# Optimization experiments

Measured on AMD Instinct MI355X. Metric: run time of the kernel, lower is better.

Reference implementation:

```python
import jax, jax.numpy as jnp
import numpy as np


def setup_inputs() -> dict:
    key = jax.random.key(0)
    k1, k2 = jax.random.split(key)
    pred = jax.random.normal(k1, (16, 4096, 3), dtype=jnp.float32)
    target = jax.random.normal(k2, (16, 4096, 3), dtype=jnp.float32)
    return {"pred": pred, "target": target}


def _pairwise_l2(pc1, pc2):
    # pc1: (B,N,3), pc2: (B,M,3) -> (B,N,M) euclidean distances (torch.cdist p=2)
    sq1 = jnp.sum(pc1 * pc1, axis=-1)  # (B,N)
    sq2 = jnp.sum(pc2 * pc2, axis=-1)  # (B,M)
    inner = jnp.einsum("bnd,bmd->bnm", pc1, pc2)  # (B,N,M)
    d2 = sq1[:, :, None] + sq2[:, None, :] - 2.0 * inner
    return jnp.sqrt(jnp.maximum(d2, 0.0))


def reference(pred, target):
    d = _pairwise_l2(pred, target)          # (B,N,M)
    dist1 = jnp.mean(jnp.min(d, axis=2), axis=1)  # (B,) pred -> target
    dist2 = jnp.mean(jnp.min(d, axis=1), axis=1)  # (B,) target -> pred
    chamfer = (dist1 + dist2) / 2.0         # bidirectional=True
    return jnp.mean(chamfer)
```

## Files before the change

### kernel.cpp

```cpp
#include <hip/hip_runtime.h>
#include <math.h>
#include <stdint.h>


#define BATCH   16
#define NPTS    4096
#define THREADS 256
#define NITEMS  (2 * BATCH * NPTS)
#define MAIN_BLOCKS (2 * BATCH * (NPTS / 128))

typedef __attribute__((ext_vector_type(8)))  _Float16 half8;
typedef __attribute__((ext_vector_type(16))) float    floatx16;

union Pack16 { float4 f4; _Float16 h[8]; half8 h8; };

__global__ __launch_bounds__(256) void chamfer_prep(
    const float* __restrict__ pred, const float* __restrict__ target,
    float4* __restrict__ packP, float4* __restrict__ packT)
{
    int g = blockIdx.x * 256 + threadIdx.x;
    int arr = g >> 16;
    int pt  = g & 65535;
    const float* src = arr ? target : pred;
    float x = src[pt * 3 + 0];
    float y = src[pt * 3 + 1];
    float z = src[pt * 3 + 2];
    _Float16 hx = (_Float16)x, hy = (_Float16)y, hz = (_Float16)z;
    float xf = (float)hx, yf = (float)hy, zf = (float)hz;
    float t = xf * xf + yf * yf + zf * zf;
    _Float16 h1 = (_Float16)t;
    _Float16 h2 = (_Float16)(t - (float)h1);
    Pack16 p;
    p.h[0] = hx; p.h[1] = hy; p.h[2] = hz; p.h[3] = h1; p.h[4] = h2;
    p.h[5] = (_Float16)0.0f; p.h[6] = (_Float16)0.0f; p.h[7] = (_Float16)0.0f;
    (arr ? packT : packP)[pt] = p.f4;
}

__device__ inline half8 make_bfrag(const Pack16& praw, bool lo) {
    half8 f;
#pragma unroll
    for (int i = 0; i < 8; ++i) f[i] = (_Float16)0.0f;
    if (lo) {
        f[0] = (_Float16)(praw.h[0] * (_Float16)-2.0f);
        f[1] = (_Float16)(praw.h[1] * (_Float16)-2.0f);
        f[2] = (_Float16)(praw.h[2] * (_Float16)-2.0f);
        f[3] = (_Float16)1.0f;
        f[4] = (_Float16)1.0f;
    }
    return f;
}

__global__ __launch_bounds__(THREADS, 4) void chamfer_main(
    const float4* __restrict__ packP, const float4* __restrict__ packT,
    float* __restrict__ blocksum)
{
    __shared__ float pmin[4][64];
    __shared__ float wsum[2];

    int tid  = threadIdx.x;
    int lane = tid & 63;
    int wave = tid >> 6;
    int qhalf = wave & 1;
    int chalf = wave >> 1;
    int l31  = lane & 31;
    bool lo  = lane < 32;

    int id = blockIdx.x;
    int ng = id & 31; id >>= 5;
    int b  = id & 15; id >>= 4;
    int dir = id;

    const float4* qpack = dir ? packT : packP;
    const float4* cpack = dir ? packP : packT;

    size_t qbase = (size_t)b * NPTS + ng * 128 + qhalf * 64;
    Pack16 prA, prB;
    prA.f4 = qpack[qbase + l31];
    prB.f4 = qpack[qbase + 32 + l31];
    half8 bfragA = make_bfrag(prA, lo);
    half8 bfragB = make_bfrag(prB, lo);

    const float4* cb = cpack + (size_t)b * NPTS + chalf * 2048;

    floatx16 zero, mnA, mnB;
#pragma unroll
    for (int r = 0; r < 16; ++r) { zero[r] = 0.0f; mnA[r] = 1e30f; mnB[r] = 1e30f; }

#pragma unroll 2
    for (int t = 0; t < 32; ++t) {
        Pack16 a0, a1;
        a0.f4 = cb[t * 64 + l31];
        a1.f4 = cb[t * 64 + 32 + l31];
        floatx16 d0 = __builtin_amdgcn_mfma_f32_32x32x16_f16(a0.h8, bfragA, zero, 0, 0, 0);
        floatx16 d1 = __builtin_amdgcn_mfma_f32_32x32x16_f16(a0.h8, bfragB, zero, 0, 0, 0);
#pragma unroll
        for (int r = 0; r < 16; ++r) mnA[r] = fminf(d0[r], mnA[r]);
#pragma unroll
        for (int r = 0; r < 16; ++r) mnB[r] = fminf(d1[r], mnB[r]);
        floatx16 d2 = __builtin_amdgcn_mfma_f32_32x32x16_f16(a1.h8, bfragA, zero, 0, 0, 0);
        floatx16 d3 = __builtin_amdgcn_mfma_f32_32x32x16_f16(a1.h8, bfragB, zero, 0, 0, 0);
#pragma unroll
        for (int r = 0; r < 16; ++r) mnA[r] = fminf(d2[r], mnA[r]);
#pragma unroll
        for (int r = 0; r < 16; ++r) mnB[r] = fminf(d3[r], mnB[r]);
    }

    float mA = fminf(fminf(fminf(mnA[0], mnA[1]),   fminf(mnA[2], mnA[3])),
                     fminf(fminf(mnA[4], mnA[5]),   fminf(mnA[6], mnA[7])));
    mA = fminf(mA, fminf(fminf(fminf(mnA[8], mnA[9]),   fminf(mnA[10], mnA[11])),
                         fminf(fminf(mnA[12], mnA[13]), fminf(mnA[14], mnA[15]))));
    float mB = fminf(fminf(fminf(mnB[0], mnB[1]),   fminf(mnB[2], mnB[3])),
                     fminf(fminf(mnB[4], mnB[5]),   fminf(mnB[6], mnB[7])));
    mB = fminf(mB, fminf(fminf(fminf(mnB[8], mnB[9]),   fminf(mnB[10], mnB[11])),
                         fminf(fminf(mnB[12], mnB[13]), fminf(mnB[14], mnB[15]))));
    mA = fminf(mA, __shfl_xor(mA, 32));
    mB = fminf(mB, __shfl_xor(mB, 32));
    if (lo) {
        pmin[wave][l31]      = mA;
        pmin[wave][l31 + 32] = mB;
    }
    __syncthreads();

    if (wave < 2) {
        float mm = fminf(pmin[wave][lane], pmin[wave + 2][lane]);
        Pack16 pr;
        pr.f4 = qpack[(size_t)b * NPTS + ng * 128 + wave * 64 + lane];
        float psq = (float)pr.h[3] + (float)pr.h[4];
        float dist = sqrtf(fmaxf(mm + psq, 0.0f));
#pragma unroll
        for (int off = 1; off <= 32; off <<= 1)
            dist += __shfl_xor(dist, off);
        if (lane == 0) wsum[wave] = dist;
    }
    __syncthreads();

    if (tid == 0)
        blocksum[blockIdx.x] = wsum[0] + wsum[1];
}

__global__ __launch_bounds__(256) void chamfer_finish(
    const float4* __restrict__ bs, float* __restrict__ out)
{
    __shared__ float ws[4];
    int tid = threadIdx.x;
    float4 v = bs[tid];
    float s = (v.x + v.y) + (v.z + v.w);
#pragma unroll
    for (int off = 1; off <= 32; off <<= 1)
        s += __shfl_xor(s, off);
    int lane = tid & 63, wave = tid >> 6;
    if (lane == 0) ws[wave] = s;
    __syncthreads();
    if (tid == 0) out[0] = (ws[0] + ws[1] + ws[2] + ws[3]) * (1.0f / (float)NITEMS);
}

extern "C" void kernel_launch(void* const* d_in, const int* in_sizes, int n_in,
                              void* d_out, int out_size, void* d_ws, size_t ws_size,
                              hipStream_t stream) {
    const float* pred   = (const float*)d_in[0];
    const float* target = (const float*)d_in[1];
    float* out = (float*)d_out;

    float4* packP = (float4*)d_ws;
    float4* packT = packP + (size_t)BATCH * NPTS;
    float*  blocksum = (float*)(packT + (size_t)BATCH * NPTS);

    chamfer_prep<<<NITEMS / 256, 256, 0, stream>>>(pred, target, packP, packT);
    chamfer_main<<<MAIN_BLOCKS, THREADS, 0, stream>>>(packP, packT, blocksum);
    chamfer_finish<<<1, 256, 0, stream>>>((const float4*)blocksum, out);
}
```

Baseline: 76.05 us.

## Halve query tile per block to 64 points and double grid size

Each block now handles 64 query points instead of 128, so every wave does two MFMAs per iteration with a single B fragment, and the grid doubles. Occupancy is raised to 8 blocks per CU through launch bounds, and the final barrier is removed by writing the block sum directly. The aim is more parallelism, better latency hiding and lower register pressure. The cost is half as much reuse of each candidate-point load, which doubles load traffic per MFMA. The finish kernel is updated to sum twice as many partials.

```diff
diff --git a/kernel.cpp b/kernel.cpp
--- a/kernel.cpp
+++ b/kernel.cpp
@@ -7,7 +7,7 @@
 #define NPTS    4096
 #define THREADS 256
 #define NITEMS  (2 * BATCH * NPTS)
-#define MAIN_BLOCKS (2 * BATCH * (NPTS / 128))
+#define MAIN_BLOCKS (2 * BATCH * (NPTS / 64))
 
 typedef __attribute__((ext_vector_type(8)))  _Float16 half8;
 typedef __attribute__((ext_vector_type(16))) float    floatx16;
@@ -50,12 +50,11 @@
     return f;
 }
 
-__global__ __launch_bounds__(THREADS, 4) void chamfer_main(
+__global__ __launch_bounds__(THREADS, 8) void chamfer_main(
     const float4* __restrict__ packP, const float4* __restrict__ packT,
     float* __restrict__ blocksum)
 {
-    __shared__ float pmin[4][64];
-    __shared__ float wsum[2];
+    __shared__ float pmin[4][32];
 
     int tid  = threadIdx.x;
     int lane = tid & 63;
@@ -66,76 +65,57 @@
     bool lo  = lane < 32;
 
     int id = blockIdx.x;
-    int ng = id & 31; id >>= 5;
+    int ng = id & 63; id >>= 6;
     int b  = id & 15; id >>= 4;
     int dir = id;
 
     const float4* qpack = dir ? packT : packP;
     const float4* cpack = dir ? packP : packT;
 
-    size_t qbase = (size_t)b * NPTS + ng * 128 + qhalf * 64;
-    Pack16 prA, prB;
+    size_t qbase = (size_t)b * NPTS + ng * 64 + qhalf * 32;
+    Pack16 prA;
     prA.f4 = qpack[qbase + l31];
-    prB.f4 = qpack[qbase + 32 + l31];
-    half8 bfragA = make_bfrag(prA, lo);
-    half8 bfragB = make_bfrag(prB, lo);
+    half8 bfrag = make_bfrag(prA, lo);
 
     const float4* cb = cpack + (size_t)b * NPTS + chalf * 2048;
 
-    floatx16 zero, mnA, mnB;
+    floatx16 zero, mn;
 #pragma unroll
-    for (int r = 0; r < 16; ++r) { zero[r] = 0.0f; mnA[r] = 1e30f; mnB[r] = 1e30f; }
+    for (int r = 0; r < 16; ++r) { zero[r] = 0.0f; mn[r] = 1e30f; }
 
 #pragma unroll 2
     for (int t = 0; t < 32; ++t) {
         Pack16 a0, a1;
         a0.f4 = cb[t * 64 + l31];
         a1.f4 = cb[t * 64 + 32 + l31];
-        floatx16 d0 = __builtin_amdgcn_mfma_f32_32x32x16_f16(a0.h8, bfragA, zero, 0, 0, 0);
-        floatx16 d1 = __builtin_amdgcn_mfma_f32_32x32x16_f16(a0.h8, bfragB, zero, 0, 0, 0);
+        floatx16 d0 = __builtin_amdgcn_mfma_f32_32x32x16_f16(a0.h8, bfrag, zero, 0, 0, 0);
+        floatx16 d1 = __builtin_amdgcn_mfma_f32_32x32x16_f16(a1.h8, bfrag, zero, 0, 0, 0);
 #pragma unroll
-        for (int r = 0; r < 16; ++r) mnA[r] = fminf(d0[r], mnA[r]);
+        for (int r = 0; r < 16; ++r) mn[r] = fminf(d0[r], mn[r]);
 #pragma unroll
-        for (int r = 0; r < 16; ++r) mnB[r] = fminf(d1[r], mnB[r]);
-        floatx16 d2 = __builtin_amdgcn_mfma_f32_32x32x16_f16(a1.h8, bfragA, zero, 0, 0, 0);
-        floatx16 d3 = __builtin_amdgcn_mfma_f32_32x32x16_f16(a1.h8, bfragB, zero, 0, 0, 0);
-#pragma unroll
-        for (int r = 0; r < 16; ++r) mnA[r] = fminf(d2[r], mnA[r]);
-#pragma unroll
-        for (int r = 0; r < 16; ++r) mnB[r] = fminf(d3[r], mnB[r]);
+        for (int r = 0; r < 16; ++r) mn[r] = fminf(d1[r], mn[r]);
     }
 
-    float mA = fminf(fminf(fminf(mnA[0], mnA[1]),   fminf(mnA[2], mnA[3])),
-                     fminf(fminf(mnA[4], mnA[5]),   fminf(mnA[6], mnA[7])));
-    mA = fminf(mA, fminf(fminf(fminf(mnA[8], mnA[9]),   fminf(mnA[10], mnA[11])),
-                         fminf(fminf(mnA[12], mnA[13]), fminf(mnA[14], mnA[15]))));
-    float mB = fminf(fminf(fminf(mnB[0], mnB[1]),   fminf(mnB[2], mnB[3])),
-                     fminf(fminf(mnB[4], mnB[5]),   fminf(mnB[6], mnB[7])));
-    mB = fminf(mB, fminf(fminf(fminf(mnB[8], mnB[9]),   fminf(mnB[10], mnB[11])),
-                         fminf(fminf(mnB[12], mnB[13]), fminf(mnB[14], mnB[15]))));
-    mA = fminf(mA, __shfl_xor(mA, 32));
-    mB = fminf(mB, __shfl_xor(mB, 32));
-    if (lo) {
-        pmin[wave][l31]      = mA;
-        pmin[wave][l31 + 32] = mB;
-    }
+    float m = fminf(fminf(fminf(mn[0], mn[1]),   fminf(mn[2], mn[3])),
+                    fminf(fminf(mn[4], mn[5]),   fminf(mn[6], mn[7])));
+    m = fminf(m, fminf(fminf(fminf(mn[8], mn[9]),   fminf(mn[10], mn[11])),
+                       fminf(fminf(mn[12], mn[13]), fminf(mn[14], mn[15]))));
+    m = fminf(m, __shfl_xor(m, 32));
+    if (lo) pmin[wave][l31] = m;
     __syncthreads();
 
-    if (wave < 2) {
-        float mm = fminf(pmin[wave][lane], pmin[wave + 2][lane]);
+    if (wave == 0) {
+        int qh = lane >> 5;
+        float mm = fminf(pmin[qh][l31], pmin[qh + 2][l31]);
         Pack16 pr;
-        pr.f4 = qpack[(size_t)b * NPTS + ng * 128 + wave * 64 + lane];
+        pr.f4 = qpack[(size_t)b * NPTS + ng * 64 + lane];
         float psq = (float)pr.h[3] + (float)pr.h[4];
         float dist = sqrtf(fmaxf(mm + psq, 0.0f));
 #pragma unroll
         for (int off = 1; off <= 32; off <<= 1)
             dist += __shfl_xor(dist, off);
-        if (lane == 0) wsum[wave] = dist;
+        if (lane == 0) blocksum[blockIdx.x] = dist;
     }
-    __syncthreads();
-
-    if (tid == 0)
-        blocksum[blockIdx.x] = wsum[0] + wsum[1];
 }
 
 __global__ __launch_bounds__(256) void chamfer_finish(
@@ -143,8 +123,9 @@
 {
     __shared__ float ws[4];
     int tid = threadIdx.x;
-    float4 v = bs[tid];
-    float s = (v.x + v.y) + (v.z + v.w);
+    float4 v0 = bs[tid];
+    float4 v1 = bs[tid + 256];
+    float s = ((v0.x + v0.y) + (v0.z + v0.w)) + ((v1.x + v1.y) + (v1.z + v1.w));
 #pragma unroll
     for (int off = 1; off <= 32; off <<= 1)
         s += __shfl_xor(s, off);
```

Result: slower. 79.41 us (+4.4%).

## Stream candidate tiles through per-wave LDS ring with async global_load_lds prefetch

Applied to the files above, without the earlier changes.

Replaces direct global loads of candidate points inside the MFMA loop with a 4-slot per-wave LDS ring buffer. Each slot is filled by global_load_lds three tiles ahead, and waits use explicit vmcnt counts. The aim is to hide global memory latency behind the MFMA and min work. In exchange it adds 16KB of LDS per block, which may limit occupancy, and relies on hand-written waitcnt ordering.

```diff
diff --git a/kernel.cpp b/kernel.cpp
--- a/kernel.cpp
+++ b/kernel.cpp
@@ -13,6 +13,11 @@
 typedef __attribute__((ext_vector_type(16))) float    floatx16;
 
 union Pack16 { float4 f4; _Float16 h[8]; half8 h8; };
+
+#define GLL(gsrc, ldst)                                                        \
+    __builtin_amdgcn_global_load_lds(                                          \
+        (const __attribute__((address_space(1))) void*)(gsrc),                 \
+        (__attribute__((address_space(3))) void*)(ldst), 16, 0, 0)
 
 __global__ __launch_bounds__(256) void chamfer_prep(
     const float* __restrict__ pred, const float* __restrict__ target,
@@ -54,6 +59,7 @@
     const float4* __restrict__ packP, const float4* __restrict__ packT,
     float* __restrict__ blocksum)
 {
+    __shared__ Pack16 ring[4][4][64];
     __shared__ float pmin[4][64];
     __shared__ float wsum[2];
 
@@ -86,24 +92,47 @@
 #pragma unroll
     for (int r = 0; r < 16; ++r) { zero[r] = 0.0f; mnA[r] = 1e30f; mnB[r] = 1e30f; }
 
-#pragma unroll 2
-    for (int t = 0; t < 32; ++t) {
-        Pack16 a0, a1;
-        a0.f4 = cb[t * 64 + l31];
-        a1.f4 = cb[t * 64 + 32 + l31];
-        floatx16 d0 = __builtin_amdgcn_mfma_f32_32x32x16_f16(a0.h8, bfragA, zero, 0, 0, 0);
-        floatx16 d1 = __builtin_amdgcn_mfma_f32_32x32x16_f16(a0.h8, bfragB, zero, 0, 0, 0);
-#pragma unroll
-        for (int r = 0; r < 16; ++r) mnA[r] = fminf(d0[r], mnA[r]);
-#pragma unroll
-        for (int r = 0; r < 16; ++r) mnB[r] = fminf(d1[r], mnB[r]);
-        floatx16 d2 = __builtin_amdgcn_mfma_f32_32x32x16_f16(a1.h8, bfragA, zero, 0, 0, 0);
-        floatx16 d3 = __builtin_amdgcn_mfma_f32_32x32x16_f16(a1.h8, bfragB, zero, 0, 0, 0);
-#pragma unroll
-        for (int r = 0; r < 16; ++r) mnA[r] = fminf(d2[r], mnA[r]);
-#pragma unroll
-        for (int r = 0; r < 16; ++r) mnB[r] = fminf(d3[r], mnB[r]);
-    }
+    GLL(cb + 0 * 64 + lane, &ring[wave][0][0]);
+    GLL(cb + 1 * 64 + lane, &ring[wave][1][0]);
+    GLL(cb + 2 * 64 + lane, &ring[wave][2][0]);
+
+#define TILE_BODY(t_)                                                          \
+    {                                                                          \
+        const Pack16* sl = &ring[wave][(t_) & 3][0];                           \
+        Pack16 a0, a1;                                                         \
+        a0.f4 = sl[l31].f4;                                                    \
+        a1.f4 = sl[32 + l31].f4;                                               \
+        floatx16 d0 = __builtin_amdgcn_mfma_f32_32x32x16_f16(a0.h8, bfragA, zero, 0, 0, 0); \
+        floatx16 d1 = __builtin_amdgcn_mfma_f32_32x32x16_f16(a0.h8, bfragB, zero, 0, 0, 0); \
+        _Pragma("unroll")                                                      \
+        for (int r = 0; r < 16; ++r) mnA[r] = fminf(d0[r], mnA[r]);            \
+        _Pragma("unroll")                                                      \
+        for (int r = 0; r < 16; ++r) mnB[r] = fminf(d1[r], mnB[r]);            \
+        floatx16 d2 = __builtin_amdgcn_mfma_f32_32x32x16_f16(a1.h8, bfragA, zero, 0, 0, 0); \
+        floatx16 d3 = __builtin_amdgcn_mfma_f32_32x32x16_f16(a1.h8, bfragB, zero, 0, 0, 0); \
+        _Pragma("unroll")                                                      \
+        for (int r = 0; r < 16; ++r) mnA[r] = fminf(d2[r], mnA[r]);            \
+        _Pragma("unroll")                                                      \
+        for (int r = 0; r < 16; ++r) mnB[r] = fminf(d3[r], mnB[r]);            \
+    }
+
+#pragma unroll 1
+    for (int t = 0; t < 29; ++t) {
+        asm volatile("s_waitcnt vmcnt(2)" ::: "memory");
+        __builtin_amdgcn_sched_barrier(0);
+        TILE_BODY(t);
+        GLL(cb + (t + 3) * 64 + lane, &ring[wave][(t + 3) & 3][0]);
+    }
+    asm volatile("s_waitcnt vmcnt(2)" ::: "memory");
+    __builtin_amdgcn_sched_barrier(0);
+    TILE_BODY(29);
+    asm volatile("s_waitcnt vmcnt(1)" ::: "memory");
+    __builtin_amdgcn_sched_barrier(0);
+    TILE_BODY(30);
+    asm volatile("s_waitcnt vmcnt(0)" ::: "memory");
+    __builtin_amdgcn_sched_barrier(0);
+    TILE_BODY(31);
+#undef TILE_BODY
 
     float mA = fminf(fminf(fminf(mnA[0], mnA[1]),   fminf(mnA[2], mnA[3])),
                      fminf(fminf(mnA[4], mnA[5]),   fminf(mnA[6], mnA[7])));
```

After: 76.49 us. Within noise of the previous version (+0.6%).
